# Kernel tuning notes

Hardware: AMD Instinct MI355X
Metric: run time of the kernel (lower is better)

## Reference

```python
import jax, jax.numpy as jnp
import numpy as np

N_NODES = 100000
N_EDGES = 1600000
IN_CH, HID_CH, OUT_CH = 128, 64, 32


def setup_inputs() -> dict:
    key = jax.random.key(0)
    k0, k1, k2, k3 = jax.random.split(key, 4)
    x = jax.random.normal(k0, (N_NODES, IN_CH), dtype=jnp.float32)
    edge_index = jax.random.randint(k1, (2, N_EDGES), 0, N_NODES, dtype=jnp.int64)
    # Glorot-style scaling for the two GCNConv weight matrices
    W1 = jax.random.normal(k2, (IN_CH, HID_CH), dtype=jnp.float32) * (2.0 / (IN_CH + HID_CH)) ** 0.5
    b1 = jnp.zeros((HID_CH,), dtype=jnp.float32)
    W2 = jax.random.normal(k3, (HID_CH, OUT_CH), dtype=jnp.float32) * (2.0 / (HID_CH + OUT_CH)) ** 0.5
    b2 = jnp.zeros((OUT_CH,), dtype=jnp.float32)
    return {"x": x, "edge_index": edge_index, "W1": W1, "b1": b1, "W2": W2, "b2": b2}


def _gcn_norm(edge_index, num_nodes):
    """Add self-loops and compute symmetric normalization deg^{-1/2}[src]*deg^{-1/2}[dst]."""
    loops = jnp.arange(num_nodes, dtype=edge_index.dtype)
    src = jnp.concatenate([edge_index[0], loops])  # message sources
    dst = jnp.concatenate([edge_index[1], loops])  # message targets
    deg = jax.ops.segment_sum(jnp.ones_like(dst, dtype=jnp.float32), dst,
                              num_segments=num_nodes)
    dinv = jnp.where(deg > 0, jax.lax.rsqrt(deg), 0.0)
    norm = dinv[src] * dinv[dst]  # [E + N]
    return src, dst, norm


def _gcn_conv(x, W, b, src, dst, norm, num_nodes):
    h = x @ W                                   # linear transform first
    msg = h[src] * norm[:, None]                # gather + scale per edge
    out = jax.ops.segment_sum(msg, dst, num_segments=num_nodes)  # scatter-add
    return out + b


def reference(x, edge_index, W1, b1, W2, b2):
    n = x.shape[0]
    src, dst, norm = _gcn_norm(edge_index, n)
    h = _gcn_conv(x, W1, b1, src, dst, norm, n)
    h = jax.nn.relu(h)
    # dropout is identity in eval mode (training=False)
    out = _gcn_conv(h, W2, b2, src, dst, norm, n)
    return out
```

## Files before the change

### kernel.cpp

```cpp
#include <hip/hip_runtime.h>

constexpr int N  = 100000;
constexpr int E  = 1600000;
constexpr int IN = 128, HID = 64, OUTC = 32;

constexpr int SHIFT = 9;
constexpr int NPB   = 1 << SHIFT;
constexpr int NB    = (N + NPB - 1) / NPB;
constexpr int CAP   = 16384;
constexpr int PB    = 800;
constexpr int CHUNK = E / PB;
constexpr int HB    = 256;

typedef __attribute__((ext_vector_type(8))) short bf16x8_t;
typedef __attribute__((ext_vector_type(4))) float f32x4_t;

__device__ __forceinline__ unsigned short f2bf(float f) {
    union { float f; unsigned int u; } v; v.f = f;
    unsigned int u = v.u;
    return (unsigned short)((u + 0x7fffu + ((u >> 16) & 1u)) >> 16);
}
__device__ __forceinline__ float blo(unsigned u) { return __uint_as_float(u << 16); }
__device__ __forceinline__ float bhi(unsigned u) { return __uint_as_float(u & 0xffff0000u); }

__global__ __launch_bounds__(256) void k_hist(const int* __restrict__ dst,
                                              int* __restrict__ gmat) {
    __shared__ int h[NB];
    for (int i = threadIdx.x; i < NB; i += 256) h[i] = 0;
    __syncthreads();
    const int tid = blockIdx.x * 256 + threadIdx.x, nt = HB * 256;
    for (int e = tid; e < E; e += nt) atomicAdd(&h[dst[e] >> SHIFT], 1);
    __syncthreads();
    for (int i = threadIdx.x; i < NB; i += 256)
        gmat[i * HB + blockIdx.x] = h[i];
}

__global__ void k_bscan(const int* __restrict__ gmat, int* __restrict__ base,
                        int* __restrict__ cursor) {
    __shared__ int sb[256];
    const int t = threadIdx.x;
    int v = 0;
    if (t < NB) {
        const int4* row = (const int4*)(gmat + t * HB);
        #pragma unroll 8
        for (int j = 0; j < HB / 4; ++j) {
            int4 a = row[j];
            v += (a.x + a.y) + (a.z + a.w);
        }
    }
    sb[t] = v; __syncthreads();
    for (int off = 1; off < 256; off <<= 1) {
        int x = (t >= off) ? sb[t - off] : 0;
        __syncthreads();
        sb[t] += x;
        __syncthreads();
    }
    if (t < NB) { int ex = sb[t] - v; base[t] = ex; cursor[t] = ex; }
    if (t == 0) base[NB] = E;
}

__global__ __launch_bounds__(256) void k_part(const int* __restrict__ src,
                                              const int* __restrict__ dst,
                                              int* __restrict__ cursor,
                                              unsigned* __restrict__ packed) {
    __shared__ int lh[NB], lb[NB], lc[NB];
    const int t = threadIdx.x;
    const int beg = blockIdx.x * CHUNK, end = beg + CHUNK;
    for (int i = t; i < NB; i += 256) lh[i] = 0;
    __syncthreads();
    for (int e = beg + t; e < end; e += 256) atomicAdd(&lh[dst[e] >> SHIFT], 1);
    __syncthreads();
    for (int i = t; i < NB; i += 256) {
        lb[i] = lh[i] ? atomicAdd(&cursor[i], lh[i]) : 0;
        lc[i] = 0;
    }
    __syncthreads();
    for (int e = beg + t; e < end; e += 256) {
        int d = dst[e], b = d >> SHIFT;
        int idx = atomicAdd(&lc[b], 1);
        packed[lb[b] + idx] = ((unsigned)(d & (NPB - 1)) << 17) | (unsigned)src[e];
    }
}

__global__ __launch_bounds__(512) void k_build(const int* __restrict__ bbase,
                                               unsigned* __restrict__ packed,
                                               int* __restrict__ offs,
                                               float* __restrict__ dinv) {
    __shared__ int cnt[NPB];
    __shared__ unsigned stage[CAP];
    const int t = threadIdx.x, b = blockIdx.x;
    const int base = bbase[b], cntE = bbase[b + 1] - base;
    const int node0 = b << SHIFT;
    cnt[t] = 0;
    __syncthreads();
    for (int i = t; i < cntE; i += 512) atomicAdd(&cnt[packed[base + i] >> 17], 1);
    __syncthreads();
    const int v = cnt[t];
    __syncthreads();
    for (int off = 1; off < NPB; off <<= 1) {
        int x = (t >= off) ? cnt[t - off] : 0;
        __syncthreads();
        cnt[t] += x;
        __syncthreads();
    }
    const int ex = cnt[t] - v;
    const int node = node0 + t;
    if (node < N) {
        offs[node] = base + ex;
        dinv[node] = rsqrtf((float)v + 1.0f);
    }
    if (node == N) offs[N] = E;
    __syncthreads();
    cnt[t] = ex;
    __syncthreads();
    for (int i = t; i < cntE; i += 512) {
        unsigned p = packed[base + i];
        int idx = atomicAdd(&cnt[p >> 17], 1);
        if (idx < CAP) stage[idx] = p & 0x1FFFFu;
    }
    __syncthreads();
    for (int i = t; i < cntE; i += 512)
        packed[base + i] = stage[i];
}

__global__ __launch_bounds__(64) void k_gemm1(const float* __restrict__ X,
                                              const float* __restrict__ W,
                                              const float* __restrict__ dinv,
                                              unsigned short* __restrict__ Hs) {
    const int l    = threadIdx.x;
    const int row0 = blockIdx.x * 16;
    const int rlo  = l & 15, khi = l >> 4;

    if (blockIdx.x == 0 && l < HID / 2)
        ((unsigned*)(Hs + (size_t)N * HID))[l] = 0u;

    const float* xrow = X + (size_t)(row0 + rlo) * IN + khi * 8;
    float4 xa[4], xb[4];
    #pragma unroll
    for (int ks = 0; ks < 4; ++ks) {
        xa[ks] = *(const float4*)(xrow + ks * 32);
        xb[ks] = *(const float4*)(xrow + ks * 32 + 4);
    }

    bf16x8_t wh[4][4], wl[4][4];
    #pragma unroll
    for (int ks = 0; ks < 4; ++ks) {
        #pragma unroll
        for (int ct = 0; ct < 4; ++ct) {
            const float* wp = W + (ks * 32 + khi * 8) * HID + ct * 16 + rlo;
            #pragma unroll
            for (int e = 0; e < 8; ++e) {
                float w = wp[e * HID];
                unsigned short h = f2bf(w);
                float r = w - __uint_as_float((unsigned)h << 16);
                wh[ks][ct][e] = (short)h;
                wl[ks][ct][e] = (short)f2bf(r);
            }
        }
    }

    f32x4_t acc[4] = {{0,0,0,0},{0,0,0,0},{0,0,0,0},{0,0,0,0}};
    #pragma unroll
    for (int ks = 0; ks < 4; ++ks) {
        float xr[8] = {xa[ks].x, xa[ks].y, xa[ks].z, xa[ks].w,
                       xb[ks].x, xb[ks].y, xb[ks].z, xb[ks].w};
        bf16x8_t ah, al;
        #pragma unroll
        for (int e = 0; e < 8; ++e) {
            unsigned short h = f2bf(xr[e]);
            ah[e] = (short)h;
            al[e] = (short)f2bf(xr[e] - __uint_as_float((unsigned)h << 16));
        }
        #pragma unroll
        for (int ct = 0; ct < 4; ++ct)
            acc[ct] = __builtin_amdgcn_mfma_f32_16x16x32_bf16(ah, wh[ks][ct], acc[ct], 0, 0, 0);
        #pragma unroll
        for (int ct = 0; ct < 4; ++ct)
            acc[ct] = __builtin_amdgcn_mfma_f32_16x16x32_bf16(al, wh[ks][ct], acc[ct], 0, 0, 0);
        #pragma unroll
        for (int ct = 0; ct < 4; ++ct)
            acc[ct] = __builtin_amdgcn_mfma_f32_16x16x32_bf16(ah, wl[ks][ct], acc[ct], 0, 0, 0);
    }

    const int orow = row0 + khi * 4;
    #pragma unroll
    for (int r = 0; r < 4; ++r) {
        const float d = dinv[orow + r];
        #pragma unroll
        for (int ct = 0; ct < 4; ++ct)
            Hs[(size_t)(orow + r) * HID + ct * 16 + rlo] = f2bf(acc[ct][r] * d);
    }
}

__global__ __launch_bounds__(256) void k_gather1f(const int* __restrict__ offs,
                                                  const int* __restrict__ csr,
                                                  const float* __restrict__ dinv,
                                                  const unsigned short* __restrict__ Hs,
                                                  const float* __restrict__ b1,
                                                  const float* __restrict__ W2,
                                                  unsigned* __restrict__ H2u) {
    __shared__ float w2s[HID * OUTC];
    __shared__ int   sidx[4][2][96];
    __shared__ float wrow[4][2][64];
    const int t = threadIdx.x;
    if (blockIdx.x == 0 && t < OUTC / 2) H2u[(size_t)N * 16 + t] = 0u;
    for (int i = t; i < HID * OUTC / 4; i += 256)
        ((float4*)w2s)[i] = ((const float4*)W2)[i];
    __syncthreads();

    const int wave = t >> 6, lane = t & 63, half = lane >> 5, c2 = lane & 31;
    const int nA = blockIdx.x * 8 + wave * 2;
    const int myNode = nA + half;
    const int o0 = offs[myNode], o1 = offs[myNode + 1];
    const int deg  = o1 - o0;
    const int rdeg = (deg + 7) & ~7;
    for (int i = c2; i < deg; i += 32) sidx[wave][half][i] = csr[o0 + i];
    if (c2 < rdeg - deg) sidx[wave][half][deg + c2] = N;

    const unsigned* __restrict__ Hu = (const unsigned*)Hs;
    const float dn = dinv[myNode];
    unsigned su = Hu[(size_t)myNode * 32 + c2];
    float ax0 = blo(su), ay0 = bhi(su);
    float ax1 = 0, ay1 = 0, ax2 = 0, ay2 = 0, ax3 = 0, ay3 = 0;
    float ax4 = 0, ay4 = 0, ax5 = 0, ay5 = 0, ax6 = 0, ay6 = 0, ax7 = 0, ay7 = 0;
    for (int k = 0; k < rdeg; k += 8) {
        int4 sa = *(const int4*)&sidx[wave][half][k];
        int4 sb = *(const int4*)&sidx[wave][half][k + 4];
        unsigned u0 = Hu[(size_t)sa.x * 32 + c2];
        unsigned u1 = Hu[(size_t)sa.y * 32 + c2];
        unsigned u2 = Hu[(size_t)sa.z * 32 + c2];
        unsigned u3 = Hu[(size_t)sa.w * 32 + c2];
        unsigned u4 = Hu[(size_t)sb.x * 32 + c2];
        unsigned u5 = Hu[(size_t)sb.y * 32 + c2];
        unsigned u6 = Hu[(size_t)sb.z * 32 + c2];
        unsigned u7 = Hu[(size_t)sb.w * 32 + c2];
        ax0 += blo(u0);  ay0 += bhi(u0);
        ax1 += blo(u1);  ay1 += bhi(u1);
        ax2 += blo(u2);  ay2 += bhi(u2);
        ax3 += blo(u3);  ay3 += bhi(u3);
        ax4 += blo(u4);  ay4 += bhi(u4);
        ax5 += blo(u5);  ay5 += bhi(u5);
        ax6 += blo(u6);  ay6 += bhi(u6);
        ax7 += blo(u7);  ay7 += bhi(u7);
    }
    float sx = ((ax0 + ax1) + (ax2 + ax3)) + ((ax4 + ax5) + (ax6 + ax7));
    float sy = ((ay0 + ay1) + (ay2 + ay3)) + ((ay4 + ay5) + (ay6 + ay7));
    float2 bb = *(const float2*)(b1 + 2 * c2);
    wrow[wave][half][2 * c2]     = fmaxf(sx * dn + bb.x, 0.0f);
    wrow[wave][half][2 * c2 + 1] = fmaxf(sy * dn + bb.y, 0.0f);

    float acc = 0.0f;
    #pragma unroll 16
    for (int k = 0; k < HID; ++k)
        acc += wrow[wave][half][k] * w2s[k * OUTC + c2];
    float hv = acc * dn;
    float hv1 = __shfl_down(hv, 1, 64);
    if ((c2 & 1) == 0)
        H2u[(size_t)myNode * 16 + (c2 >> 1)] =
            (unsigned)f2bf(hv) | ((unsigned)f2bf(hv1) << 16);
}

__global__ __launch_bounds__(256) void k_gather2(const int* __restrict__ offs,
                                                 const int* __restrict__ csr,
                                                 const float* __restrict__ dinv,
                                                 const unsigned* __restrict__ H2u,
                                                 const float* __restrict__ b2,
                                                 float* __restrict__ out) {
    __shared__ int sidx[4][4][96];
    const int t = threadIdx.x;
    const int wave = t >> 6, lane = t & 63, q = lane >> 4, c2 = lane & 15;
    const int n0 = blockIdx.x * 16 + wave * 4;
    const int myNode = n0 + q;
    const int o0 = offs[myNode], o1 = offs[myNode + 1];
    const int deg  = o1 - o0;
    const int rdeg = (deg + 7) & ~7;
    for (int i = c2; i < deg; i += 16) sidx[wave][q][i] = csr[o0 + i];
    if (c2 < rdeg - deg) sidx[wave][q][deg + c2] = N;

    const float dn = dinv[myNode];
    unsigned su = H2u[(size_t)myNode * 16 + c2];
    float ax0 = blo(su), ay0 = bhi(su);
    float ax1 = 0, ay1 = 0, ax2 = 0, ay2 = 0, ax3 = 0, ay3 = 0;
    float ax4 = 0, ay4 = 0, ax5 = 0, ay5 = 0, ax6 = 0, ay6 = 0, ax7 = 0, ay7 = 0;
    for (int k = 0; k < rdeg; k += 8) {
        int4 sa = *(const int4*)&sidx[wave][q][k];
        int4 sb = *(const int4*)&sidx[wave][q][k + 4];
        unsigned u0 = H2u[(size_t)sa.x * 16 + c2];
        unsigned u1 = H2u[(size_t)sa.y * 16 + c2];
        unsigned u2 = H2u[(size_t)sa.z * 16 + c2];
        unsigned u3 = H2u[(size_t)sa.w * 16 + c2];
        unsigned u4 = H2u[(size_t)sb.x * 16 + c2];
        unsigned u5 = H2u[(size_t)sb.y * 16 + c2];
        unsigned u6 = H2u[(size_t)sb.z * 16 + c2];
        unsigned u7 = H2u[(size_t)sb.w * 16 + c2];
        ax0 += blo(u0);  ay0 += bhi(u0);
        ax1 += blo(u1);  ay1 += bhi(u1);
        ax2 += blo(u2);  ay2 += bhi(u2);
        ax3 += blo(u3);  ay3 += bhi(u3);
        ax4 += blo(u4);  ay4 += bhi(u4);
        ax5 += blo(u5);  ay5 += bhi(u5);
        ax6 += blo(u6);  ay6 += bhi(u6);
        ax7 += blo(u7);  ay7 += bhi(u7);
    }
    float sx = ((ax0 + ax1) + (ax2 + ax3)) + ((ax4 + ax5) + (ax6 + ax7));
    float sy = ((ay0 + ay1) + (ay2 + ay3)) + ((ay4 + ay5) + (ay6 + ay7));
    float2 bb = *(const float2*)(b2 + 2 * c2);
    float2 r;
    r.x = sx * dn + bb.x;
    r.y = sy * dn + bb.y;
    *(float2*)(out + (size_t)myNode * OUTC + 2 * c2) = r;
}

extern "C" void kernel_launch(void* const* d_in, const int* in_sizes, int n_in,
                              void* d_out, int out_size, void* d_ws, size_t ws_size,
                              hipStream_t stream) {
    const float* x   = (const float*)d_in[0];
    const int*   ei  = (const int*)d_in[1];
    const float* W1  = (const float*)d_in[2];
    const float* b1  = (const float*)d_in[3];
    const float* W2  = (const float*)d_in[4];
    const float* b2  = (const float*)d_in[5];
    float*       out = (float*)d_out;

    const int* srcp = ei;
    const int* dstp = ei + E;

    char* ws = (char*)d_ws;
    int*            bbase  = (int*)(ws + 4096);
    int*            cursor = (int*)(ws + 8192);
    int*            offs   = (int*)(ws + 16384);
    float*          dinv   = (float*)(ws + (512u << 10));
    unsigned*       packed = (unsigned*)(ws + (1u << 20));
    unsigned short* Hs     = (unsigned short*)(ws + (8u << 20));
    unsigned*       H2u    = (unsigned*)(ws + (21u << 20));
    int*            csr    = (int*)packed;
    int*            gmat   = (int*)Hs;

    k_hist <<<HB, 256, 0, stream>>>(dstp, gmat);
    k_bscan<<<1, 256, 0, stream>>>(gmat, bbase, cursor);
    k_part <<<PB, 256, 0, stream>>>(srcp, dstp, cursor, packed);
    k_build<<<NB, 512, 0, stream>>>(bbase, packed, offs, dinv);

    k_gemm1   <<<N / 16, 64,  0, stream>>>(x, W1, dinv, Hs);
    k_gather1f<<<N / 8,  256, 0, stream>>>(offs, csr, dinv, Hs, b1, W2, H2u);
    k_gather2 <<<N / 16, 256, 0, stream>>>(offs, csr, dinv, H2u, b2, out);
}
```

Measured before the change: 232.3 us.

## Amortize W1 split across row tiles and widen gather loads to 8 bytes

```diff
diff --git a/kernel.cpp b/kernel.cpp
--- a/kernel.cpp
+++ b/kernel.cpp
@@ -11,6 +11,7 @@
 constexpr int PB    = 800;
 constexpr int CHUNK = E / PB;
 constexpr int HB    = 256;
+constexpr int G1T   = 5;
 
 typedef __attribute__((ext_vector_type(8))) short bf16x8_t;
 typedef __attribute__((ext_vector_type(4))) float f32x4_t;
@@ -128,18 +129,20 @@
                                               const float* __restrict__ dinv,
                                               unsigned short* __restrict__ Hs) {
     const int l    = threadIdx.x;
-    const int row0 = blockIdx.x * 16;
     const int rlo  = l & 15, khi = l >> 4;
+    const int base = blockIdx.x * (16 * G1T);
 
     if (blockIdx.x == 0 && l < HID / 2)
         ((unsigned*)(Hs + (size_t)N * HID))[l] = 0u;
 
-    const float* xrow = X + (size_t)(row0 + rlo) * IN + khi * 8;
     float4 xa[4], xb[4];
-    #pragma unroll
-    for (int ks = 0; ks < 4; ++ks) {
-        xa[ks] = *(const float4*)(xrow + ks * 32);
-        xb[ks] = *(const float4*)(xrow + ks * 32 + 4);
+    {
+        const float* xr = X + (size_t)(base + rlo) * IN + khi * 8;
+        #pragma unroll
+        for (int ks = 0; ks < 4; ++ks) {
+            xa[ks] = *(const float4*)(xr + ks * 32);
+            xb[ks] = *(const float4*)(xr + ks * 32 + 4);
+        }
     }
 
     bf16x8_t wh[4][4], wl[4][4];
@@ -159,36 +162,52 @@
         }
     }
 
-    f32x4_t acc[4] = {{0,0,0,0},{0,0,0,0},{0,0,0,0},{0,0,0,0}};
     #pragma unroll
-    for (int ks = 0; ks < 4; ++ks) {
-        float xr[8] = {xa[ks].x, xa[ks].y, xa[ks].z, xa[ks].w,
-                       xb[ks].x, xb[ks].y, xb[ks].z, xb[ks].w};
-        bf16x8_t ah, al;
-        #pragma unroll
-        for (int e = 0; e < 8; ++e) {
-            unsigned short h = f2bf(xr[e]);
-            ah[e] = (short)h;
-            al[e] = (short)f2bf(xr[e] - __uint_as_float((unsigned)h << 16));
-        }
-        #pragma unroll
-        for (int ct = 0; ct < 4; ++ct)
-            acc[ct] = __builtin_amdgcn_mfma_f32_16x16x32_bf16(ah, wh[ks][ct], acc[ct], 0, 0, 0);
-        #pragma unroll
-        for (int ct = 0; ct < 4; ++ct)
-            acc[ct] = __builtin_amdgcn_mfma_f32_16x16x32_bf16(al, wh[ks][ct], acc[ct], 0, 0, 0);
-        #pragma unroll
-        for (int ct = 0; ct < 4; ++ct)
-            acc[ct] = __builtin_amdgcn_mfma_f32_16x16x32_bf16(ah, wl[ks][ct], acc[ct], 0, 0, 0);
-    }
-
-    const int orow = row0 + khi * 4;
-    #pragma unroll
-    for (int r = 0; r < 4; ++r) {
-        const float d = dinv[orow + r];
-        #pragma unroll
-        for (int ct = 0; ct < 4; ++ct)
-            Hs[(size_t)(orow + r) * HID + ct * 16 + rlo] = f2bf(acc[ct][r] * d);
+    for (int tile = 0; tile < G1T; ++tile) {
+        const int row0 = base + tile * 16;
+        float4 cxa[4], cxb[4];
+        #pragma unroll
+        for (int ks = 0; ks < 4; ++ks) { cxa[ks] = xa[ks]; cxb[ks] = xb[ks]; }
+        if (tile + 1 < G1T) {
+            const float* xr = X + (size_t)(row0 + 16 + rlo) * IN + khi * 8;
+            #pragma unroll
+            for (int ks = 0; ks < 4; ++ks) {
+                xa[ks] = *(const float4*)(xr + ks * 32);
+                xb[ks] = *(const float4*)(xr + ks * 32 + 4);
+            }
+        }
+
+        f32x4_t acc[4] = {{0,0,0,0},{0,0,0,0},{0,0,0,0},{0,0,0,0}};
+        #pragma unroll
+        for (int ks = 0; ks < 4; ++ks) {
+            float xr8[8] = {cxa[ks].x, cxa[ks].y, cxa[ks].z, cxa[ks].w,
+                            cxb[ks].x, cxb[ks].y, cxb[ks].z, cxb[ks].w};
+            bf16x8_t ah, al;
+            #pragma unroll
+            for (int e = 0; e < 8; ++e) {
+                unsigned short h = f2bf(xr8[e]);
+                ah[e] = (short)h;
+                al[e] = (short)f2bf(xr8[e] - __uint_as_float((unsigned)h << 16));
+            }
+            #pragma unroll
+            for (int ct = 0; ct < 4; ++ct)
+                acc[ct] = __builtin_amdgcn_mfma_f32_16x16x32_bf16(ah, wh[ks][ct], acc[ct], 0, 0, 0);
+            #pragma unroll
+            for (int ct = 0; ct < 4; ++ct)
+                acc[ct] = __builtin_amdgcn_mfma_f32_16x16x32_bf16(al, wh[ks][ct], acc[ct], 0, 0, 0);
+            #pragma unroll
+            for (int ct = 0; ct < 4; ++ct)
+                acc[ct] = __builtin_amdgcn_mfma_f32_16x16x32_bf16(ah, wl[ks][ct], acc[ct], 0, 0, 0);
+        }
+
+        const int orow = row0 + khi * 4;
+        #pragma unroll
+        for (int r = 0; r < 4; ++r) {
+            const float d = dinv[orow + r];
+            #pragma unroll
+            for (int ct = 0; ct < 4; ++ct)
+                Hs[(size_t)(orow + r) * HID + ct * 16 + rlo] = f2bf(acc[ct][r] * d);
+        }
     }
 }
 
@@ -200,64 +219,69 @@
                                                   const float* __restrict__ W2,
                                                   unsigned* __restrict__ H2u) {
     __shared__ float w2s[HID * OUTC];
-    __shared__ int   sidx[4][2][96];
-    __shared__ float wrow[4][2][64];
+    __shared__ int   sidx[4][4][96];
+    __shared__ float wrow[4][4][64];
     const int t = threadIdx.x;
     if (blockIdx.x == 0 && t < OUTC / 2) H2u[(size_t)N * 16 + t] = 0u;
     for (int i = t; i < HID * OUTC / 4; i += 256)
         ((float4*)w2s)[i] = ((const float4*)W2)[i];
     __syncthreads();
 
-    const int wave = t >> 6, lane = t & 63, half = lane >> 5, c2 = lane & 31;
-    const int nA = blockIdx.x * 8 + wave * 2;
-    const int myNode = nA + half;
+    const int wave = t >> 6, lane = t & 63, q = lane >> 4, c = lane & 15;
+    const int myNode = blockIdx.x * 16 + wave * 4 + q;
     const int o0 = offs[myNode], o1 = offs[myNode + 1];
     const int deg  = o1 - o0;
     const int rdeg = (deg + 7) & ~7;
-    for (int i = c2; i < deg; i += 32) sidx[wave][half][i] = csr[o0 + i];
-    if (c2 < rdeg - deg) sidx[wave][half][deg + c2] = N;
-
-    const unsigned* __restrict__ Hu = (const unsigned*)Hs;
+    for (int i = c; i < deg; i += 16) sidx[wave][q][i] = csr[o0 + i];
+    if (c < rdeg - deg) sidx[wave][q][deg + c] = N;
+
+    const uint2* __restrict__ Hu2 = (const uint2*)Hs;
     const float dn = dinv[myNode];
-    unsigned su = Hu[(size_t)myNode * 32 + c2];
-    float ax0 = blo(su), ay0 = bhi(su);
-    float ax1 = 0, ay1 = 0, ax2 = 0, ay2 = 0, ax3 = 0, ay3 = 0;
-    float ax4 = 0, ay4 = 0, ax5 = 0, ay5 = 0, ax6 = 0, ay6 = 0, ax7 = 0, ay7 = 0;
+    uint2 su = Hu2[(size_t)myNode * 16 + c];
+    float p0 = blo(su.x), p1 = bhi(su.x), p2 = blo(su.y), p3 = bhi(su.y);
+    float r0 = 0, r1 = 0, r2 = 0, r3 = 0;
     for (int k = 0; k < rdeg; k += 8) {
-        int4 sa = *(const int4*)&sidx[wave][half][k];
-        int4 sb = *(const int4*)&sidx[wave][half][k + 4];
-        unsigned u0 = Hu[(size_t)sa.x * 32 + c2];
-        unsigned u1 = Hu[(size_t)sa.y * 32 + c2];
-        unsigned u2 = Hu[(size_t)sa.z * 32 + c2];
-        unsigned u3 = Hu[(size_t)sa.w * 32 + c2];
-        unsigned u4 = Hu[(size_t)sb.x * 32 + c2];
-        unsigned u5 = Hu[(size_t)sb.y * 32 + c2];
-        unsigned u6 = Hu[(size_t)sb.z * 32 + c2];
-        unsigned u7 = Hu[(size_t)sb.w * 32 + c2];
-        ax0 += blo(u0);  ay0 += bhi(u0);
-        ax1 += blo(u1);  ay1 += bhi(u1);
-        ax2 += blo(u2);  ay2 += bhi(u2);
-        ax3 += blo(u3);  ay3 += bhi(u3);
-        ax4 += blo(u4);  ay4 += bhi(u4);
-        ax5 += blo(u5);  ay5 += bhi(u5);
-        ax6 += blo(u6);  ay6 += bhi(u6);
-        ax7 += blo(u7);  ay7 += bhi(u7);
-    }
-    float sx = ((ax0 + ax1) + (ax2 + ax3)) + ((ax4 + ax5) + (ax6 + ax7));
-    float sy = ((ay0 + ay1) + (ay2 + ay3)) + ((ay4 + ay5) + (ay6 + ay7));
-    float2 bb = *(const float2*)(b1 + 2 * c2);
-    wrow[wave][half][2 * c2]     = fmaxf(sx * dn + bb.x, 0.0f);
-    wrow[wave][half][2 * c2 + 1] = fmaxf(sy * dn + bb.y, 0.0f);
-
-    float acc = 0.0f;
-    #pragma unroll 16
-    for (int k = 0; k < HID; ++k)
-        acc += wrow[wave][half][k] * w2s[k * OUTC + c2];
-    float hv = acc * dn;
-    float hv1 = __shfl_down(hv, 1, 64);
-    if ((c2 & 1) == 0)
-        H2u[(size_t)myNode * 16 + (c2 >> 1)] =
-            (unsigned)f2bf(hv) | ((unsigned)f2bf(hv1) << 16);
+        int4 sa = *(const int4*)&sidx[wave][q][k];
+        int4 sb = *(const int4*)&sidx[wave][q][k + 4];
+        uint2 u0 = Hu2[(size_t)sa.x * 16 + c];
+        uint2 u1 = Hu2[(size_t)sa.y * 16 + c];
+        uint2 u2 = Hu2[(size_t)sa.z * 16 + c];
+        uint2 u3 = Hu2[(size_t)sa.w * 16 + c];
+        uint2 u4 = Hu2[(size_t)sb.x * 16 + c];
+        uint2 u5 = Hu2[(size_t)sb.y * 16 + c];
+        uint2 u6 = Hu2[(size_t)sb.z * 16 + c];
+        uint2 u7 = Hu2[(size_t)sb.w * 16 + c];
+        p0 += blo(u0.x); p1 += bhi(u0.x); p2 += blo(u0.y); p3 += bhi(u0.y);
+        r0 += blo(u1.x); r1 += bhi(u1.x); r2 += blo(u1.y); r3 += bhi(u1.y);
+        p0 += blo(u2.x); p1 += bhi(u2.x); p2 += blo(u2.y); p3 += bhi(u2.y);
+        r0 += blo(u3.x); r1 += bhi(u3.x); r2 += blo(u3.y); r3 += bhi(u3.y);
+        p0 += blo(u4.x); p1 += bhi(u4.x); p2 += blo(u4.y); p3 += bhi(u4.y);
+        r0 += blo(u5.x); r1 += bhi(u5.x); r2 += blo(u5.y); r3 += bhi(u5.y);
+        p0 += blo(u6.x); p1 += bhi(u6.x); p2 += blo(u6.y); p3 += bhi(u6.y);
+        r0 += blo(u7.x); r1 += bhi(u7.x); r2 += blo(u7.y); r3 += bhi(u7.y);
+    }
+    float s0 = p0 + r0, s1 = p1 + r1, s2 = p2 + r2, s3 = p3 + r3;
+    float4 bb = *(const float4*)(b1 + 4 * c);
+    float4 wv;
+    wv.x = fmaxf(s0 * dn + bb.x, 0.0f);
+    wv.y = fmaxf(s1 * dn + bb.y, 0.0f);
+    wv.z = fmaxf(s2 * dn + bb.z, 0.0f);
+    wv.w = fmaxf(s3 * dn + bb.w, 0.0f);
+    *(float4*)&wrow[wave][q][4 * c] = wv;
+
+    float acc0 = 0.0f, acc1 = 0.0f;
+    #pragma unroll
+    for (int k = 0; k < HID; k += 4) {
+        float4 wr = *(const float4*)&wrow[wave][q][k];
+        float2 wa = *(const float2*)&w2s[(k + 0) * OUTC + 2 * c];
+        float2 wb = *(const float2*)&w2s[(k + 1) * OUTC + 2 * c];
+        float2 wc = *(const float2*)&w2s[(k + 2) * OUTC + 2 * c];
+        float2 wd = *(const float2*)&w2s[(k + 3) * OUTC + 2 * c];
+        acc0 += wr.x * wa.x + wr.y * wb.x + wr.z * wc.x + wr.w * wd.x;
+        acc1 += wr.x * wa.y + wr.y * wb.y + wr.z * wc.y + wr.w * wd.y;
+    }
+    H2u[(size_t)myNode * 16 + c] =
+        (unsigned)f2bf(acc0 * dn) | ((unsigned)f2bf(acc1 * dn) << 16);
 }
 
 __global__ __launch_bounds__(256) void k_gather2(const int* __restrict__ offs,
@@ -266,49 +290,49 @@
                                                  const unsigned* __restrict__ H2u,
                                                  const float* __restrict__ b2,
                                                  float* __restrict__ out) {
-    __shared__ int sidx[4][4][96];
+    __shared__ int sidx[4][8][96];
     const int t = threadIdx.x;
-    const int wave = t >> 6, lane = t & 63, q = lane >> 4, c2 = lane & 15;
-    const int n0 = blockIdx.x * 16 + wave * 4;
-    const int myNode = n0 + q;
+    const int wave = t >> 6, lane = t & 63, q = lane >> 3, c = lane & 7;
+    const int myNode = blockIdx.x * 32 + wave * 8 + q;
     const int o0 = offs[myNode], o1 = offs[myNode + 1];
     const int deg  = o1 - o0;
     const int rdeg = (deg + 7) & ~7;
-    for (int i = c2; i < deg; i += 16) sidx[wave][q][i] = csr[o0 + i];
-    if (c2 < rdeg - deg) sidx[wave][q][deg + c2] = N;
-
+    for (int i = c; i < deg; i += 8) sidx[wave][q][i] = csr[o0 + i];
+    if (c < rdeg - deg) sidx[wave][q][deg + c] = N;
+
+    const uint2* __restrict__ H2 = (const uint2*)H2u;
     const float dn = dinv[myNode];
-    unsigned su = H2u[(size_t)myNode * 16 + c2];
-    float ax0 = blo(su), ay0 = bhi(su);
-    float ax1 = 0, ay1 = 0, ax2 = 0, ay2 = 0, ax3 = 0, ay3 = 0;
-    float ax4 = 0, ay4 = 0, ax5 = 0, ay5 = 0, ax6 = 0, ay6 = 0, ax7 = 0, ay7 = 0;
+    uint2 su = H2[(size_t)myNode * 8 + c];
+    float p0 = blo(su.x), p1 = bhi(su.x), p2 = blo(su.y), p3 = bhi(su.y);
+    float r0 = 0, r1 = 0, r2 = 0, r3 = 0;
     for (int k = 0; k < rdeg; k += 8) {
         int4 sa = *(const int4*)&sidx[wave][q][k];
         int4 sb = *(const int4*)&sidx[wave][q][k + 4];
-        unsigned u0 = H2u[(size_t)sa.x * 16 + c2];
-        unsigned u1 = H2u[(size_t)sa.y * 16 + c2];
-        unsigned u2 = H2u[(size_t)sa.z * 16 + c2];
-        unsigned u3 = H2u[(size_t)sa.w * 16 + c2];
-        unsigned u4 = H2u[(size_t)sb.x * 16 + c2];
-        unsigned u5 = H2u[(size_t)sb.y * 16 + c2];
-        unsigned u6 = H2u[(size_t)sb.z * 16 + c2];
-        unsigned u7 = H2u[(size_t)sb.w * 16 + c2];
-        ax0 += blo(u0);  ay0 += bhi(u0);
-        ax1 += blo(u1);  ay1 += bhi(u1);
-        ax2 += blo(u2);  ay2 += bhi(u2);
-        ax3 += blo(u3);  ay3 += bhi(u3);
-        ax4 += blo(u4);  ay4 += bhi(u4);
-        ax5 += blo(u5);  ay5 += bhi(u5);
-        ax6 += blo(u6);  ay6 += bhi(u6);
-        ax7 += blo(u7);  ay7 += bhi(u7);
-    }
-    float sx = ((ax0 + ax1) + (ax2 + ax3)) + ((ax4 + ax5) + (ax6 + ax7));
-    float sy = ((ay0 + ay1) + (ay2 + ay3)) + ((ay4 + ay5) + (ay6 + ay7));
-    float2 bb = *(const float2*)(b2 + 2 * c2);
-    float2 r;
-    r.x = sx * dn + bb.x;
-    r.y = sy * dn + bb.y;
-    *(float2*)(out + (size_t)myNode * OUTC + 2 * c2) = r;
+        uint2 u0 = H2[(size_t)sa.x * 8 + c];
+        uint2 u1 = H2[(size_t)sa.y * 8 + c];
+        uint2 u2 = H2[(size_t)sa.z * 8 + c];
+        uint2 u3 = H2[(size_t)sa.w * 8 + c];
+        uint2 u4 = H2[(size_t)sb.x * 8 + c];
+        uint2 u5 = H2[(size_t)sb.y * 8 + c];
+        uint2 u6 = H2[(size_t)sb.z * 8 + c];
+        uint2 u7 = H2[(size_t)sb.w * 8 + c];
+        p0 += blo(u0.x); p1 += bhi(u0.x); p2 += blo(u0.y); p3 += bhi(u0.y);
+        r0 += blo(u1.x); r1 += bhi(u1.x); r2 += blo(u1.y); r3 += bhi(u1.y);
+        p0 += blo(u2.x); p1 += bhi(u2.x); p2 += blo(u2.y); p3 += bhi(u2.y);
+        r0 += blo(u3.x); r1 += bhi(u3.x); r2 += blo(u3.y); r3 += bhi(u3.y);
+        p0 += blo(u4.x); p1 += bhi(u4.x); p2 += blo(u4.y); p3 += bhi(u4.y);
+        r0 += blo(u5.x); r1 += bhi(u5.x); r2 += blo(u5.y); r3 += bhi(u5.y);
+        p0 += blo(u6.x); p1 += bhi(u6.x); p2 += blo(u6.y); p3 += bhi(u6.y);
+        r0 += blo(u7.x); r1 += bhi(u7.x); r2 += blo(u7.y); r3 += bhi(u7.y);
+    }
+    float s0 = p0 + r0, s1 = p1 + r1, s2 = p2 + r2, s3 = p3 + r3;
+    float4 bb = *(const float4*)(b2 + 4 * c);
+    float4 r;
+    r.x = s0 * dn + bb.x;
+    r.y = s1 * dn + bb.y;
+    r.z = s2 * dn + bb.z;
+    r.w = s3 * dn + bb.w;
+    *(float4*)(out + (size_t)myNode * OUTC + 4 * c) = r;
 }
 
 extern "C" void kernel_launch(void* const* d_in, const int* in_sizes, int n_in,
@@ -341,7 +365,7 @@
     k_part <<<PB, 256, 0, stream>>>(srcp, dstp, cursor, packed);
     k_build<<<NB, 512, 0, stream>>>(bbase, packed, offs, dinv);
 
-    k_gemm1   <<<N / 16, 64,  0, stream>>>(x, W1, dinv, Hs);
-    k_gather1f<<<N / 8,  256, 0, stream>>>(offs, csr, dinv, Hs, b1, W2, H2u);
-    k_gather2 <<<N / 16, 256, 0, stream>>>(offs, csr, dinv, H2u, b2, out);
-}
+    k_gemm1   <<<N / (16 * G1T), 64, 0, stream>>>(x, W1, dinv, Hs);
+    k_gather1f<<<N / 16, 256, 0, stream>>>(offs, csr, dinv, Hs, b1, W2, H2u);
+    k_gather2 <<<N / 32, 256, 0, stream>>>(offs, csr, dinv, H2u, b2, out);
+}
```

After: 225.1 us. 3.1% less time.
